# Kernel optimization log

Hardware: AMD Instinct MI355X
Metric: run time of the kernel (lower is better)

Reference implementation:

```python
import jax, jax.numpy as jnp
import numpy as np

DIM = 1024   # dim
T = 16       # maximum_time_steps
NT = 64      # num_templates
B = 2048     # batch
S = 77       # words per sentence


def setup_inputs() -> dict:
    key = jax.random.key(0)
    ks = jax.random.split(key, 16)
    p = lambda k, shp: jax.random.normal(k, shp, dtype=jnp.float32) * 0.02
    return {
        "text_feats": jax.random.normal(ks[0], (B, S, DIM), dtype=jnp.float32),
        "text_sentence_feats": jax.random.normal(ks[1], (B, DIM), dtype=jnp.float32),
        "textual_query": jax.random.normal(ks[2], (B, DIM), dtype=jnp.float32),
        "time_step": jax.random.randint(ks[3], (B,), 0, T),
        "W1_w": p(ks[4], (T, DIM, DIM)),   # T stacked [out,in] linears
        "W1_b": p(ks[5], (T, DIM)),
        "W2_w": p(ks[6], (DIM, 2 * DIM)),
        "W2_b": p(ks[7], (DIM,)),
        "m1_w": p(ks[8], (DIM, DIM)),
        "m1_b": p(ks[9], (DIM,)),
        "m2_w": p(ks[10], (DIM, DIM)),
        "m2_b": p(ks[11], (DIM,)),
        "m3_w": p(ks[12], (NT, DIM)),
        "m3_b": p(ks[13], (NT,)),
        "attn_w": p(ks[14], (1, DIM)),
        "attn_b": p(ks[15], (1,)),
    }


def reference(text_feats, text_sentence_feats, textual_query, time_step,
              W1_w, W1_b, W2_w, W2_b, m1_w, m1_b, m2_w, m2_b, m3_w, m3_b,
              attn_w, attn_b):
    # Time-indexed linear: T is small, so compute all T projections for every
    # sample and select per-sample (avoids materializing a [B,DIM,DIM] gather).
    all_proj = jnp.einsum('bc,toc->tbo', text_sentence_feats, W1_w) + W1_b[:, None, :]  # t b d
    x1 = jnp.take_along_axis(all_proj, time_step[None, :, None], axis=0)[0]  # b d
    # concat with textual query, project back to dim
    x = jnp.concatenate([x1, textual_query], axis=-1) @ W2_w.T + W2_b  # b d
    # 3-layer MLP -> template distribution
    h = jax.nn.relu(x @ m1_w.T + m1_b)
    h = jax.nn.relu(h @ m2_w.T + m2_b)
    template_distribution = jax.nn.softmax(h @ m3_w.T + m3_b, axis=-1)  # b #templates
    # soft attention over words: score each (x * word_feat) with a linear
    x_w = x[:, None, :] * text_feats  # b s c
    scores = jnp.einsum('bsc,c->bs', x_w, attn_w[0]) + attn_b[0]
    words_soft_distribution = jax.nn.softmax(scores, axis=-1)  # b s
    c_t = jnp.einsum('bs,bsc->bc', words_soft_distribution, text_feats)  # b c
    return template_distribution, words_soft_distribution, c_t
```

## Files before the change

### kernel.cpp

```cpp
#include <hip/hip_runtime.h>
#include <stdint.h>

typedef __bf16 bf16;
typedef bf16 bf16x8 __attribute__((ext_vector_type(8)));
typedef bf16 bf16x4 __attribute__((ext_vector_type(4)));
typedef float f32x4 __attribute__((ext_vector_type(4)));

#define DIM   1024
#define TMAX  16
#define NTPL  64
#define BATCH 2048
#define SLEN  77

__device__ __forceinline__ void gl_lds16(const void* g, void* l) {
  __builtin_amdgcn_global_load_lds(
      (const __attribute__((address_space(1))) void*)g,
      (__attribute__((address_space(3))) void*)l, 16, 0, 0);
}

__global__ void bucket_k(const int* __restrict__ ts, int* __restrict__ perm,
                         int* __restrict__ bstart) {
  __shared__ int cnt[TMAX], base[TMAX], cur[TMAX];
  int tid = threadIdx.x;
  if (tid < TMAX) { cnt[tid] = 0; cur[tid] = 0; }
  __syncthreads();
  for (int b = tid; b < BATCH; b += 256) atomicAdd(&cnt[ts[b]], 1);
  __syncthreads();
  if (tid == 0) {
    int a = 0;
    for (int t = 0; t < TMAX; ++t) { base[t] = a; bstart[t] = a; a += cnt[t]; }
    bstart[TMAX] = a;
  }
  __syncthreads();
  for (int b = tid; b < BATCH; b += 256) {
    int t = ts[b];
    perm[base[t] + atomicAdd(&cur[t], 1)] = b;
  }
}

__global__ void cvt_bf16_k(const float* __restrict__ src, bf16* __restrict__ dst) {
  int idx = blockIdx.x * 256 + threadIdx.x;
  float4 v = ((const float4*)src)[idx];
  bf16x4 o = {(bf16)v.x, (bf16)v.y, (bf16)v.z, (bf16)v.w};
  ((bf16x4*)dst)[idx] = o;
}

__global__ void cvt_tq_k(const float* __restrict__ tq, bf16* __restrict__ xcat) {
  int idx = blockIdx.x * 256 + threadIdx.x;
  int b = idx >> 8, c4 = idx & 255;
  float4 v = ((const float4*)(tq + (size_t)b * DIM))[c4];
  bf16x4 o = {(bf16)v.x, (bf16)v.y, (bf16)v.z, (bf16)v.w};
  *(bf16x4*)(xcat + (size_t)b * 2 * DIM + DIM + c4 * 4) = o;
}

__global__ __launch_bounds__(256, 4) void gemm_bt64(
    const bf16* __restrict__ A, int lda, const bf16* __restrict__ B, int ldb,
    const float* __restrict__ bias, bf16* __restrict__ C, int ldc,
    float* __restrict__ Cf, int N, int K, int relu) {
  __shared__ bf16 As[2][64 * 32];
  __shared__ bf16 Bs[2][64 * 32];
  const int tid = threadIdx.x;
  const int rowBase = blockIdx.y * 64, colBase = blockIdx.x * 64;

  const int r = tid >> 2, kq = tid & 3;
  const bf16* ag = A + (size_t)(rowBase + r) * lda + kq * 8;
  int bn = colBase + r; if (bn > N - 1) bn = N - 1;
  const bf16* bg = B + (size_t)bn * ldb + kq * 8;

  const int wave = tid >> 6, lane = tid & 63;
  const int wm = wave >> 1, wn = wave & 1;
  const int mr = lane & 15, quad = lane >> 4;

  f32x4 acc[2][2];
#pragma unroll
  for (int i = 0; i < 2; ++i)
#pragma unroll
    for (int j = 0; j < 2; ++j) acc[i][j] = (f32x4){0.f, 0.f, 0.f, 0.f};

  gl_lds16(ag, &As[0][tid * 8]);
  gl_lds16(bg, &Bs[0][tid * 8]);
  __syncthreads();

  const int nk = K >> 5;
  for (int t = 0; t < nk; ++t) {
    const int cur = t & 1;
    if (t + 1 < nk) {
      gl_lds16(ag + (t + 1) * 32, &As[cur ^ 1][tid * 8]);
      gl_lds16(bg + (t + 1) * 32, &Bs[cur ^ 1][tid * 8]);
    }
    bf16x8 af[2], bfr[2];
#pragma unroll
    for (int i = 0; i < 2; ++i)
      af[i] = *(const bf16x8*)&As[cur][(wm * 32 + i * 16 + mr) * 32 + quad * 8];
#pragma unroll
    for (int j = 0; j < 2; ++j)
      bfr[j] = *(const bf16x8*)&Bs[cur][(wn * 32 + j * 16 + mr) * 32 + quad * 8];
#pragma unroll
    for (int i = 0; i < 2; ++i)
#pragma unroll
      for (int j = 0; j < 2; ++j)
        acc[i][j] = __builtin_amdgcn_mfma_f32_16x16x32_bf16(af[i], bfr[j], acc[i][j], 0, 0, 0);
    __syncthreads();
  }

  const int r0 = quad * 4;
#pragma unroll
  for (int i = 0; i < 2; ++i) {
    int gm = rowBase + wm * 32 + i * 16 + r0;
#pragma unroll
    for (int j = 0; j < 2; ++j) {
      int gn = colBase + wn * 32 + j * 16 + mr;
      if (gn < N) {
        float bv = bias ? bias[gn] : 0.f;
#pragma unroll
        for (int rr = 0; rr < 4; ++rr) {
          float v = acc[i][j][rr] + bv;
          if (relu) v = fmaxf(v, 0.f);
          C[(size_t)(gm + rr) * ldc + gn] = (bf16)v;
          if (Cf) Cf[(size_t)(gm + rr) * ldc + gn] = v;
        }
      }
    }
  }
}

__global__ __launch_bounds__(256, 4) void gemm_stage1(
    const bf16* __restrict__ tsbf, const bf16* __restrict__ W1bf,
    const float* __restrict__ W1b, const int* __restrict__ perm,
    const int* __restrict__ bstart, bf16* __restrict__ xcat) {
  const int t = blockIdx.z;
  const int s0 = bstart[t];
  const int cnt = bstart[t + 1] - s0;
  const int by = blockIdx.y;
  if (by * 64 >= cnt) return;
  __shared__ bf16 As[2][64 * 32];
  __shared__ bf16 Bs[2][64 * 32];
  const int tid = threadIdx.x;
  const int colBase = blockIdx.x * 64;
  const bf16* Bmat = W1bf + ((size_t)t << 20);

  const int r = tid >> 2, kq = tid & 3;
  const int lr0 = by * 64 + r;
  const int src = perm[s0 + (lr0 < cnt ? lr0 : 0)];
  const bf16* ag = tsbf + (size_t)src * DIM + kq * 8;
  const bf16* bg = Bmat + (size_t)(colBase + r) * DIM + kq * 8;

  const int wave = tid >> 6, lane = tid & 63;
  const int wm = wave >> 1, wn = wave & 1;
  const int mr = lane & 15, quad = lane >> 4;

  f32x4 acc[2][2];
#pragma unroll
  for (int i = 0; i < 2; ++i)
#pragma unroll
    for (int j = 0; j < 2; ++j) acc[i][j] = (f32x4){0.f, 0.f, 0.f, 0.f};

  gl_lds16(ag, &As[0][tid * 8]);
  gl_lds16(bg, &Bs[0][tid * 8]);
  __syncthreads();

  const int nk = DIM >> 5;
  for (int t2 = 0; t2 < nk; ++t2) {
    const int cur = t2 & 1;
    if (t2 + 1 < nk) {
      gl_lds16(ag + (t2 + 1) * 32, &As[cur ^ 1][tid * 8]);
      gl_lds16(bg + (t2 + 1) * 32, &Bs[cur ^ 1][tid * 8]);
    }
    bf16x8 af[2], bfr[2];
#pragma unroll
    for (int i = 0; i < 2; ++i)
      af[i] = *(const bf16x8*)&As[cur][(wm * 32 + i * 16 + mr) * 32 + quad * 8];
#pragma unroll
    for (int j = 0; j < 2; ++j)
      bfr[j] = *(const bf16x8*)&Bs[cur][(wn * 32 + j * 16 + mr) * 32 + quad * 8];
#pragma unroll
    for (int i = 0; i < 2; ++i)
#pragma unroll
      for (int j = 0; j < 2; ++j)
        acc[i][j] = __builtin_amdgcn_mfma_f32_16x16x32_bf16(af[i], bfr[j], acc[i][j], 0, 0, 0);
    __syncthreads();
  }

  const int r0 = quad * 4;
#pragma unroll
  for (int i = 0; i < 2; ++i) {
    int lr = by * 64 + wm * 32 + i * 16 + r0;
#pragma unroll
    for (int j = 0; j < 2; ++j) {
      int gn = colBase + wn * 32 + j * 16 + mr;
      float bv = W1b[t * DIM + gn];
#pragma unroll
      for (int rr = 0; rr < 4; ++rr) {
        if (lr + rr < cnt) {
          int bidx = perm[s0 + lr + rr];
          xcat[(size_t)bidx * 2 * DIM + gn] = (bf16)(acc[i][j][rr] + bv);
        }
      }
    }
  }
}

__global__ __launch_bounds__(256) void softmax64_k(const bf16* __restrict__ logits,
                                                   float* __restrict__ out) {
  int row = blockIdx.x * 4 + (threadIdx.x >> 6);
  int lane = threadIdx.x & 63;
  float v = (float)logits[row * NTPL + lane];
  float mx = v;
#pragma unroll
  for (int o = 32; o; o >>= 1) mx = fmaxf(mx, __shfl_xor(mx, o));
  float e = __expf(v - mx);
  float s = e;
#pragma unroll
  for (int o = 32; o; o >>= 1) s += __shfl_xor(s, o);
  out[row * NTPL + lane] = e / s;
}

__global__ __launch_bounds__(256) void attn_k(
    const float* __restrict__ x, const float* __restrict__ attn_w,
    const float* __restrict__ attn_b, const float* __restrict__ feats,
    float* __restrict__ words, float* __restrict__ ct) {
  const int b = blockIdx.x;
  const int tid = threadIdx.x;
  const int wave = tid >> 6, lane = tid & 63;
  const float* fb = feats + (size_t)b * SLEN * DIM;

  float4 vj[4];
#pragma unroll
  for (int j = 0; j < 4; ++j) {
    int d = 4 * lane + 256 * j;
    float4 xv = *(const float4*)(x + (size_t)b * DIM + d);
    float4 aw = *(const float4*)(attn_w + d);
    vj[j] = make_float4(xv.x * aw.x, xv.y * aw.y, xv.z * aw.z, xv.w * aw.w);
  }
  const float ab = attn_b[0];

  __shared__ float s_acc[4][DIM];
  __shared__ float s_m[4], s_l[4], s_sc[SLEN];

  float m = -1e30f, l = 0.f;
  float4 acc[4];
#pragma unroll
  for (int j = 0; j < 4; ++j) acc[j] = make_float4(0.f, 0.f, 0.f, 0.f);

  float4 f[4];
  {
    const float* fr = fb + (size_t)wave * DIM;
#pragma unroll
    for (int j = 0; j < 4; ++j) f[j] = *(const float4*)(fr + 4 * lane + 256 * j);
  }

  for (int s = wave; s < SLEN; s += 4) {
    float4 fn[4];
    if (s + 4 < SLEN) {
      const float* fr = fb + (size_t)(s + 4) * DIM;
#pragma unroll
      for (int j = 0; j < 4; ++j) fn[j] = *(const float4*)(fr + 4 * lane + 256 * j);
    }
    float p = 0.f;
#pragma unroll
    for (int j = 0; j < 4; ++j)
      p += f[j].x * vj[j].x + f[j].y * vj[j].y + f[j].z * vj[j].z + f[j].w * vj[j].w;
#pragma unroll
    for (int o = 32; o; o >>= 1) p += __shfl_xor(p, o);
    float score = p + ab;
    if (lane == 0) s_sc[s] = score;

    float mn = fmaxf(m, score);
    float scale = __expf(m - mn);
    float w = __expf(score - mn);
    l = l * scale + w;
#pragma unroll
    for (int j = 0; j < 4; ++j) {
      acc[j].x = acc[j].x * scale + w * f[j].x;
      acc[j].y = acc[j].y * scale + w * f[j].y;
      acc[j].z = acc[j].z * scale + w * f[j].z;
      acc[j].w = acc[j].w * scale + w * f[j].w;
    }
    m = mn;
    if (s + 4 < SLEN) {
#pragma unroll
      for (int j = 0; j < 4; ++j) f[j] = fn[j];
    }
  }

#pragma unroll
  for (int j = 0; j < 4; ++j)
    *(float4*)&s_acc[wave][4 * lane + 256 * j] = acc[j];
  if (lane == 0) { s_m[wave] = m; s_l[wave] = l; }
  __syncthreads();

  const float gm = fmaxf(fmaxf(s_m[0], s_m[1]), fmaxf(s_m[2], s_m[3]));
  float sc0 = __expf(s_m[0] - gm), sc1 = __expf(s_m[1] - gm);
  float sc2 = __expf(s_m[2] - gm), sc3 = __expf(s_m[3] - gm);
  const float L = s_l[0] * sc0 + s_l[1] * sc1 + s_l[2] * sc2 + s_l[3] * sc3;
  const float inv = 1.f / L;

  float4 a0 = *(const float4*)&s_acc[0][4 * tid];
  float4 a1 = *(const float4*)&s_acc[1][4 * tid];
  float4 a2 = *(const float4*)&s_acc[2][4 * tid];
  float4 a3 = *(const float4*)&s_acc[3][4 * tid];
  float4 o;
  o.x = (a0.x * sc0 + a1.x * sc1 + a2.x * sc2 + a3.x * sc3) * inv;
  o.y = (a0.y * sc0 + a1.y * sc1 + a2.y * sc2 + a3.y * sc3) * inv;
  o.z = (a0.z * sc0 + a1.z * sc1 + a2.z * sc2 + a3.z * sc3) * inv;
  o.w = (a0.w * sc0 + a1.w * sc1 + a2.w * sc2 + a3.w * sc3) * inv;
  ((float4*)(ct + (size_t)b * DIM))[tid] = o;

  if (tid < SLEN) words[(size_t)b * SLEN + tid] = __expf(s_sc[tid] - gm) * inv;
}

extern "C" void kernel_launch(void* const* d_in, const int* in_sizes, int n_in,
                              void* d_out, int out_size, void* d_ws, size_t ws_size,
                              hipStream_t stream) {
  const float* feats = (const float*)d_in[0];
  const float* tsent = (const float*)d_in[1];
  const float* tq    = (const float*)d_in[2];
  const int*   tstep = (const int*)d_in[3];
  const float* W1w = (const float*)d_in[4];
  const float* W1b = (const float*)d_in[5];
  const float* W2w = (const float*)d_in[6];
  const float* W2b = (const float*)d_in[7];
  const float* m1w = (const float*)d_in[8];
  const float* m1b = (const float*)d_in[9];
  const float* m2w = (const float*)d_in[10];
  const float* m2b = (const float*)d_in[11];
  const float* m3w = (const float*)d_in[12];
  const float* m3b = (const float*)d_in[13];
  const float* attw = (const float*)d_in[14];
  const float* attb = (const float*)d_in[15];

  char* p = (char*)d_ws;
  auto alloc = [&](size_t bytes) { char* q = p; p += (bytes + 255) & ~(size_t)255; return q; };
  int*  perm   = (int*)alloc(BATCH * 4);
  int*  bstart = (int*)alloc(17 * 4);
  bf16* tsbf = (bf16*)alloc((size_t)BATCH * DIM * 2);
  bf16* W1bf = (bf16*)alloc((size_t)TMAX * DIM * DIM * 2);
  bf16* W2bf = (bf16*)alloc((size_t)DIM * 2 * DIM * 2);
  bf16* m1bf = (bf16*)alloc((size_t)DIM * DIM * 2);
  bf16* m2bf = (bf16*)alloc((size_t)DIM * DIM * 2);
  bf16* m3bf = (bf16*)alloc((size_t)NTPL * DIM * 2);
  bf16* xcat = (bf16*)alloc((size_t)BATCH * 2 * DIM * 2);
  bf16* xbf  = (bf16*)alloc((size_t)BATCH * DIM * 2);
  float* xf  = (float*)alloc((size_t)BATCH * DIM * 4);
  bf16* h1   = (bf16*)alloc((size_t)BATCH * DIM * 2);
  bf16* h2   = (bf16*)alloc((size_t)BATCH * DIM * 2);
  bf16* lg   = (bf16*)alloc((size_t)BATCH * NTPL * 2);

  float* out_td = (float*)d_out;
  float* out_w  = out_td + (size_t)BATCH * NTPL;
  float* out_ct = out_w + (size_t)BATCH * SLEN;

  bucket_k<<<1, 256, 0, stream>>>(tstep, perm, bstart);
  cvt_bf16_k<<<(TMAX * DIM * DIM) / 1024, 256, 0, stream>>>(W1w, W1bf);
  cvt_bf16_k<<<(BATCH * DIM) / 1024, 256, 0, stream>>>(tsent, tsbf);
  cvt_bf16_k<<<(DIM * 2 * DIM) / 1024, 256, 0, stream>>>(W2w, W2bf);
  cvt_bf16_k<<<(DIM * DIM) / 1024, 256, 0, stream>>>(m1w, m1bf);
  cvt_bf16_k<<<(DIM * DIM) / 1024, 256, 0, stream>>>(m2w, m2bf);
  cvt_bf16_k<<<(NTPL * DIM) / 1024, 256, 0, stream>>>(m3w, m3bf);
  cvt_tq_k<<<(BATCH * DIM) / 1024, 256, 0, stream>>>(tq, xcat);

  gemm_stage1<<<dim3(DIM / 64, BATCH / 64, TMAX), 256, 0, stream>>>(
      tsbf, W1bf, W1b, perm, bstart, xcat);
  gemm_bt64<<<dim3(DIM / 64, BATCH / 64), 256, 0, stream>>>(
      xcat, 2 * DIM, W2bf, 2 * DIM, W2b, xbf, DIM, xf, DIM, 2 * DIM, 0);
  gemm_bt64<<<dim3(DIM / 64, BATCH / 64), 256, 0, stream>>>(
      xbf, DIM, m1bf, DIM, m1b, h1, DIM, nullptr, DIM, DIM, 1);
  gemm_bt64<<<dim3(DIM / 64, BATCH / 64), 256, 0, stream>>>(
      h1, DIM, m2bf, DIM, m2b, h2, DIM, nullptr, DIM, DIM, 1);
  gemm_bt64<<<dim3(1, BATCH / 64), 256, 0, stream>>>(
      h2, DIM, m3bf, DIM, m3b, lg, NTPL, nullptr, NTPL, DIM, 0);
  softmax64_k<<<BATCH / 4, 256, 0, stream>>>(lg, out_td);
  attn_k<<<BATCH, 256, 0, stream>>>(xf, attw, attb, feats, out_w, out_ct);
}
```

Before: 1.022 ms.

## Merge prep kernels, deepen GEMM pipeline to 4 stages, fuse m3 GEMM with softmax

```diff
diff --git a/kernel.cpp b/kernel.cpp
--- a/kernel.cpp
+++ b/kernel.cpp
@@ -18,47 +18,106 @@
       (__attribute__((address_space(3))) void*)l, 16, 0, 0);
 }
 
-__global__ void bucket_k(const int* __restrict__ ts, int* __restrict__ perm,
-                         int* __restrict__ bstart) {
-  __shared__ int cnt[TMAX], base[TMAX], cur[TMAX];
-  int tid = threadIdx.x;
-  if (tid < TMAX) { cnt[tid] = 0; cur[tid] = 0; }
-  __syncthreads();
-  for (int b = tid; b < BATCH; b += 256) atomicAdd(&cnt[ts[b]], 1);
-  __syncthreads();
-  if (tid == 0) {
-    int a = 0;
-    for (int t = 0; t < TMAX; ++t) { base[t] = a; bstart[t] = a; a += cnt[t]; }
-    bstart[TMAX] = a;
-  }
-  __syncthreads();
-  for (int b = tid; b < BATCH; b += 256) {
-    int t = ts[b];
-    perm[base[t] + atomicAdd(&cur[t], 1)] = b;
-  }
-}
-
-__global__ void cvt_bf16_k(const float* __restrict__ src, bf16* __restrict__ dst) {
-  int idx = blockIdx.x * 256 + threadIdx.x;
-  float4 v = ((const float4*)src)[idx];
-  bf16x4 o = {(bf16)v.x, (bf16)v.y, (bf16)v.z, (bf16)v.w};
-  ((bf16x4*)dst)[idx] = o;
-}
-
-__global__ void cvt_tq_k(const float* __restrict__ tq, bf16* __restrict__ xcat) {
-  int idx = blockIdx.x * 256 + threadIdx.x;
-  int b = idx >> 8, c4 = idx & 255;
-  float4 v = ((const float4*)(tq + (size_t)b * DIM))[c4];
-  bf16x4 o = {(bf16)v.x, (bf16)v.y, (bf16)v.z, (bf16)v.w};
-  *(bf16x4*)(xcat + (size_t)b * 2 * DIM + DIM + c4 * 4) = o;
+__global__ void prep_k(const float* __restrict__ W1w, bf16* __restrict__ W1bf,
+                       const float* __restrict__ tsent, bf16* __restrict__ tsbf,
+                       const float* __restrict__ W2w, bf16* __restrict__ W2bf,
+                       const float* __restrict__ m1w, bf16* __restrict__ m1bf,
+                       const float* __restrict__ m2w, bf16* __restrict__ m2bf,
+                       const float* __restrict__ m3w, bf16* __restrict__ m3bf,
+                       const float* __restrict__ tq, bf16* __restrict__ xcat,
+                       const int* __restrict__ ts, int* __restrict__ perm,
+                       int* __restrict__ bstart) {
+  const int blk = blockIdx.x;
+  const int tid = threadIdx.x;
+  if (blk < 22592) {
+    const float* src; bf16* dst; int base;
+    if (blk < 16384)      { src = W1w;   dst = W1bf; base = blk; }
+    else if (blk < 18432) { src = tsent; dst = tsbf; base = blk - 16384; }
+    else if (blk < 20480) { src = W2w;   dst = W2bf; base = blk - 18432; }
+    else if (blk < 21504) { src = m1w;   dst = m1bf; base = blk - 20480; }
+    else if (blk < 22528) { src = m2w;   dst = m2bf; base = blk - 21504; }
+    else                  { src = m3w;   dst = m3bf; base = blk - 22528; }
+    int idx = base * 256 + tid;
+    float4 v = ((const float4*)src)[idx];
+    bf16x4 o = {(bf16)v.x, (bf16)v.y, (bf16)v.z, (bf16)v.w};
+    ((bf16x4*)dst)[idx] = o;
+  } else if (blk < 24640) {
+    int idx = (blk - 22592) * 256 + tid;
+    int b = idx >> 8, c4 = idx & 255;
+    float4 v = ((const float4*)(tq + (size_t)b * DIM))[c4];
+    bf16x4 o = {(bf16)v.x, (bf16)v.y, (bf16)v.z, (bf16)v.w};
+    *(bf16x4*)(xcat + (size_t)b * 2 * DIM + DIM + c4 * 4) = o;
+  } else {
+    __shared__ int cnt[TMAX], base_s[TMAX], cur[TMAX];
+    if (tid < TMAX) { cnt[tid] = 0; cur[tid] = 0; }
+    __syncthreads();
+    for (int b = tid; b < BATCH; b += 256) atomicAdd(&cnt[ts[b]], 1);
+    __syncthreads();
+    if (tid == 0) {
+      int a = 0;
+      for (int t = 0; t < TMAX; ++t) { base_s[t] = a; bstart[t] = a; a += cnt[t]; }
+      bstart[TMAX] = a;
+    }
+    __syncthreads();
+    for (int b = tid; b < BATCH; b += 256) {
+      int t = ts[b];
+      perm[base_s[t] + atomicAdd(&cur[t], 1)] = b;
+    }
+  }
+}
+
+__device__ __forceinline__ void gemm_pipe(
+    bf16 (*As)[64 * 32], bf16 (*Bs)[64 * 32],
+    const bf16* ag, const bf16* bg, int nk, int tid,
+    int wm, int wn, int mr, int quad, f32x4 (&acc)[2][2]) {
+  auto stage = [&](int t) {
+    int buf = t & 3;
+    gl_lds16(ag + t * 32, &As[buf][tid * 8]);
+    gl_lds16(bg + t * 32, &Bs[buf][tid * 8]);
+  };
+  auto compute = [&](int t) {
+    int buf = t & 3;
+    bf16x8 af[2], bfr[2];
+#pragma unroll
+    for (int i = 0; i < 2; ++i)
+      af[i] = *(const bf16x8*)&As[buf][(wm * 32 + i * 16 + mr) * 32 + quad * 8];
+#pragma unroll
+    for (int j = 0; j < 2; ++j)
+      bfr[j] = *(const bf16x8*)&Bs[buf][(wn * 32 + j * 16 + mr) * 32 + quad * 8];
+#pragma unroll
+    for (int i = 0; i < 2; ++i)
+#pragma unroll
+      for (int j = 0; j < 2; ++j)
+        acc[i][j] = __builtin_amdgcn_mfma_f32_16x16x32_bf16(af[i], bfr[j], acc[i][j], 0, 0, 0);
+  };
+  stage(0);
+  stage(1);
+  for (int t = 0; t < nk - 2; ++t) {
+    stage(t + 2);
+    asm volatile("s_waitcnt vmcnt(4)" ::: "memory");
+    __builtin_amdgcn_sched_barrier(0);
+    __builtin_amdgcn_s_barrier();
+    __builtin_amdgcn_sched_barrier(0);
+    compute(t);
+  }
+  asm volatile("s_waitcnt vmcnt(2)" ::: "memory");
+  __builtin_amdgcn_sched_barrier(0);
+  __builtin_amdgcn_s_barrier();
+  __builtin_amdgcn_sched_barrier(0);
+  compute(nk - 2);
+  asm volatile("s_waitcnt vmcnt(0)" ::: "memory");
+  __builtin_amdgcn_sched_barrier(0);
+  __builtin_amdgcn_s_barrier();
+  __builtin_amdgcn_sched_barrier(0);
+  compute(nk - 1);
 }
 
 __global__ __launch_bounds__(256, 4) void gemm_bt64(
     const bf16* __restrict__ A, int lda, const bf16* __restrict__ B, int ldb,
     const float* __restrict__ bias, bf16* __restrict__ C, int ldc,
     float* __restrict__ Cf, int N, int K, int relu) {
-  __shared__ bf16 As[2][64 * 32];
-  __shared__ bf16 Bs[2][64 * 32];
+  __shared__ bf16 As[4][64 * 32];
+  __shared__ bf16 Bs[4][64 * 32];
   const int tid = threadIdx.x;
   const int rowBase = blockIdx.y * 64, colBase = blockIdx.x * 64;
 
@@ -77,31 +136,7 @@
 #pragma unroll
     for (int j = 0; j < 2; ++j) acc[i][j] = (f32x4){0.f, 0.f, 0.f, 0.f};
 
-  gl_lds16(ag, &As[0][tid * 8]);
-  gl_lds16(bg, &Bs[0][tid * 8]);
-  __syncthreads();
-
-  const int nk = K >> 5;
-  for (int t = 0; t < nk; ++t) {
-    const int cur = t & 1;
-    if (t + 1 < nk) {
-      gl_lds16(ag + (t + 1) * 32, &As[cur ^ 1][tid * 8]);
-      gl_lds16(bg + (t + 1) * 32, &Bs[cur ^ 1][tid * 8]);
-    }
-    bf16x8 af[2], bfr[2];
-#pragma unroll
-    for (int i = 0; i < 2; ++i)
-      af[i] = *(const bf16x8*)&As[cur][(wm * 32 + i * 16 + mr) * 32 + quad * 8];
-#pragma unroll
-    for (int j = 0; j < 2; ++j)
-      bfr[j] = *(const bf16x8*)&Bs[cur][(wn * 32 + j * 16 + mr) * 32 + quad * 8];
-#pragma unroll
-    for (int i = 0; i < 2; ++i)
-#pragma unroll
-      for (int j = 0; j < 2; ++j)
-        acc[i][j] = __builtin_amdgcn_mfma_f32_16x16x32_bf16(af[i], bfr[j], acc[i][j], 0, 0, 0);
-    __syncthreads();
-  }
+  gemm_pipe(As, Bs, ag, bg, K >> 5, tid, wm, wn, mr, quad, acc);
 
   const int r0 = quad * 4;
 #pragma unroll
@@ -133,8 +168,8 @@
   const int cnt = bstart[t + 1] - s0;
   const int by = blockIdx.y;
   if (by * 64 >= cnt) return;
-  __shared__ bf16 As[2][64 * 32];
-  __shared__ bf16 Bs[2][64 * 32];
+  __shared__ bf16 As[4][64 * 32];
+  __shared__ bf16 Bs[4][64 * 32];
   const int tid = threadIdx.x;
   const int colBase = blockIdx.x * 64;
   const bf16* Bmat = W1bf + ((size_t)t << 20);
@@ -155,31 +190,7 @@
 #pragma unroll
     for (int j = 0; j < 2; ++j) acc[i][j] = (f32x4){0.f, 0.f, 0.f, 0.f};
 
-  gl_lds16(ag, &As[0][tid * 8]);
-  gl_lds16(bg, &Bs[0][tid * 8]);
-  __syncthreads();
-
-  const int nk = DIM >> 5;
-  for (int t2 = 0; t2 < nk; ++t2) {
-    const int cur = t2 & 1;
-    if (t2 + 1 < nk) {
-      gl_lds16(ag + (t2 + 1) * 32, &As[cur ^ 1][tid * 8]);
-      gl_lds16(bg + (t2 + 1) * 32, &Bs[cur ^ 1][tid * 8]);
-    }
-    bf16x8 af[2], bfr[2];
-#pragma unroll
-    for (int i = 0; i < 2; ++i)
-      af[i] = *(const bf16x8*)&As[cur][(wm * 32 + i * 16 + mr) * 32 + quad * 8];
-#pragma unroll
-    for (int j = 0; j < 2; ++j)
-      bfr[j] = *(const bf16x8*)&Bs[cur][(wn * 32 + j * 16 + mr) * 32 + quad * 8];
-#pragma unroll
-    for (int i = 0; i < 2; ++i)
-#pragma unroll
-      for (int j = 0; j < 2; ++j)
-        acc[i][j] = __builtin_amdgcn_mfma_f32_16x16x32_bf16(af[i], bfr[j], acc[i][j], 0, 0, 0);
-    __syncthreads();
-  }
+  gemm_pipe(As, Bs, ag, bg, DIM >> 5, tid, wm, wn, mr, quad, acc);
 
   const int r0 = quad * 4;
 #pragma unroll
@@ -200,19 +211,56 @@
   }
 }
 
-__global__ __launch_bounds__(256) void softmax64_k(const bf16* __restrict__ logits,
-                                                   float* __restrict__ out) {
-  int row = blockIdx.x * 4 + (threadIdx.x >> 6);
-  int lane = threadIdx.x & 63;
-  float v = (float)logits[row * NTPL + lane];
-  float mx = v;
-#pragma unroll
-  for (int o = 32; o; o >>= 1) mx = fmaxf(mx, __shfl_xor(mx, o));
-  float e = __expf(v - mx);
-  float s = e;
-#pragma unroll
-  for (int o = 32; o; o >>= 1) s += __shfl_xor(s, o);
-  out[row * NTPL + lane] = e / s;
+__global__ __launch_bounds__(256) void gemm_m3sm(
+    const bf16* __restrict__ A, const bf16* __restrict__ B,
+    const float* __restrict__ bias, float* __restrict__ out) {
+  __shared__ bf16 As[4][64 * 32];
+  __shared__ bf16 Bs[4][64 * 32];
+  __shared__ float ls[64][65];
+  const int tid = threadIdx.x;
+  const int rowBase = blockIdx.x * 64;
+
+  const int r = tid >> 2, kq = tid & 3;
+  const bf16* ag = A + (size_t)(rowBase + r) * DIM + kq * 8;
+  const bf16* bg = B + (size_t)r * DIM + kq * 8;
+
+  const int wave = tid >> 6, lane = tid & 63;
+  const int wm = wave >> 1, wn = wave & 1;
+  const int mr = lane & 15, quad = lane >> 4;
+
+  f32x4 acc[2][2];
+#pragma unroll
+  for (int i = 0; i < 2; ++i)
+#pragma unroll
+    for (int j = 0; j < 2; ++j) acc[i][j] = (f32x4){0.f, 0.f, 0.f, 0.f};
+
+  gemm_pipe(As, Bs, ag, bg, DIM >> 5, tid, wm, wn, mr, quad, acc);
+
+  const int r0 = quad * 4;
+#pragma unroll
+  for (int i = 0; i < 2; ++i)
+#pragma unroll
+    for (int j = 0; j < 2; ++j) {
+      int gn = wn * 32 + j * 16 + mr;
+      float bv = bias[gn];
+#pragma unroll
+      for (int rr = 0; rr < 4; ++rr)
+        ls[wm * 32 + i * 16 + r0 + rr][gn] = acc[i][j][rr] + bv;
+    }
+  __syncthreads();
+#pragma unroll
+  for (int rr2 = 0; rr2 < 16; ++rr2) {
+    int row = wave * 16 + rr2;
+    float v = ls[row][lane];
+    float mx = v;
+#pragma unroll
+    for (int o = 32; o; o >>= 1) mx = fmaxf(mx, __shfl_xor(mx, o));
+    float e = __expf(v - mx);
+    float s = e;
+#pragma unroll
+    for (int o = 32; o; o >>= 1) s += __shfl_xor(s, o);
+    out[(size_t)(rowBase + row) * NTPL + lane] = e / s;
+  }
 }
 
 __global__ __launch_bounds__(256) void attn_k(
@@ -344,21 +392,14 @@
   float* xf  = (float*)alloc((size_t)BATCH * DIM * 4);
   bf16* h1   = (bf16*)alloc((size_t)BATCH * DIM * 2);
   bf16* h2   = (bf16*)alloc((size_t)BATCH * DIM * 2);
-  bf16* lg   = (bf16*)alloc((size_t)BATCH * NTPL * 2);
 
   float* out_td = (float*)d_out;
   float* out_w  = out_td + (size_t)BATCH * NTPL;
   float* out_ct = out_w + (size_t)BATCH * SLEN;
 
-  bucket_k<<<1, 256, 0, stream>>>(tstep, perm, bstart);
-  cvt_bf16_k<<<(TMAX * DIM * DIM) / 1024, 256, 0, stream>>>(W1w, W1bf);
-  cvt_bf16_k<<<(BATCH * DIM) / 1024, 256, 0, stream>>>(tsent, tsbf);
-  cvt_bf16_k<<<(DIM * 2 * DIM) / 1024, 256, 0, stream>>>(W2w, W2bf);
-  cvt_bf16_k<<<(DIM * DIM) / 1024, 256, 0, stream>>>(m1w, m1bf);
-  cvt_bf16_k<<<(DIM * DIM) / 1024, 256, 0, stream>>>(m2w, m2bf);
-  cvt_bf16_k<<<(NTPL * DIM) / 1024, 256, 0, stream>>>(m3w, m3bf);
-  cvt_tq_k<<<(BATCH * DIM) / 1024, 256, 0, stream>>>(tq, xcat);
-
+  prep_k<<<24641, 256, 0, stream>>>(W1w, W1bf, tsent, tsbf, W2w, W2bf,
+                                    m1w, m1bf, m2w, m2bf, m3w, m3bf,
+                                    tq, xcat, tstep, perm, bstart);
   gemm_stage1<<<dim3(DIM / 64, BATCH / 64, TMAX), 256, 0, stream>>>(
       tsbf, W1bf, W1b, perm, bstart, xcat);
   gemm_bt64<<<dim3(DIM / 64, BATCH / 64), 256, 0, stream>>>(
@@ -367,8 +408,6 @@
       xbf, DIM, m1bf, DIM, m1b, h1, DIM, nullptr, DIM, DIM, 1);
   gemm_bt64<<<dim3(DIM / 64, BATCH / 64), 256, 0, stream>>>(
       h1, DIM, m2bf, DIM, m2b, h2, DIM, nullptr, DIM, DIM, 1);
-  gemm_bt64<<<dim3(1, BATCH / 64), 256, 0, stream>>>(
-      h2, DIM, m3bf, DIM, m3b, lg, NTPL, nullptr, NTPL, DIM, 0);
-  softmax64_k<<<BATCH / 4, 256, 0, stream>>>(lg, out_td);
+  gemm_m3sm<<<BATCH / 64, 256, 0, stream>>>(h2, m3bf, m3b, out_td);
   attn_k<<<BATCH, 256, 0, stream>>>(xf, attw, attb, feats, out_w, out_ct);
 }
```

After: 992.1 us. 1.03x faster.
